# Kernel tuning notes

Hardware: AMD Instinct MI355X
Metric: run time of the kernel (lower is better)

Reference implementation:

```python
import jax, jax.numpy as jnp
import numpy as np

N_NODES = 50000
N_EDGES = 800000
LN_EPS = 1e-5


def _segment_softmax_aggr(msg, t, dst, n):
    # SoftmaxAggregation(learn=True): alpha = softmax(msg * t) per dest segment, out = sum(alpha * msg)
    logits = msg * t  # [E, C]
    m = jax.ops.segment_max(logits, dst, num_segments=n)
    m = jnp.where(jnp.isfinite(m), m, 0.0)  # empty segments -> 0 to keep exp finite
    e = jnp.exp(logits - m[dst])
    denom = jax.ops.segment_sum(e, dst, num_segments=n)
    alpha = e / jnp.maximum(denom[dst], 1e-16)
    return jax.ops.segment_sum(alpha * msg, dst, num_segments=n)


def _sage_conv(x, src, dst, wp, bp, t, wl, bl, wr):
    # project=True: messages come from relu(lin(x)); root term uses ORIGINAL x
    xp = jax.nn.relu(x @ wp + bp)
    msg = xp[src]                                   # [E, C] gather
    aggr = _segment_softmax_aggr(msg, t, dst, x.shape[0])
    out = aggr @ wl + bl + x @ wr
    # normalize=True: L2 normalize rows (eps as in F.normalize)
    nrm = jnp.maximum(jnp.linalg.norm(out, axis=-1, keepdims=True), 1e-12)
    return out / nrm


def _mem_pool(x, k, w_conv, wl, bl):
    # PyG MemPooling, tau=1: Student-t kernel 1/(1+d^2)
    H, K, F = k.shape
    kk = k.reshape(H * K, F)
    d2 = (jnp.sum(kk * kk, -1)[:, None] + jnp.sum(x * x, -1)[None, :]
          - 2.0 * kk @ x.T)                          # [H*K, N]
    d2 = jnp.maximum(d2, 0.0)
    dist = 1.0 / (1.0 + d2)
    dist = dist.reshape(H, K, -1).transpose(0, 2, 1)  # [H, N, K]
    S = dist / jnp.sum(dist, -1, keepdims=True)       # per-head normalize over clusters
    S = jnp.einsum('h,hnk->nk', w_conv, S)            # 1x1 conv mixing heads (no bias)
    S = jax.nn.softmax(S, axis=-1)                    # [N, K]
    xp = S.T @ x                                      # [K, F]
    return xp @ wl + bl                               # [K, out]


def setup_inputs() -> dict:
    key = jax.random.key(0)
    ks = jax.random.split(key, 20)
    rn = lambda i, shp, s: jax.random.normal(ks[i], shp, dtype=jnp.float32) * s
    inp = {
        'x': rn(0, (N_NODES, 64), 1.0),
        'edge_index': jax.random.randint(ks[1], (2, N_EDGES), 0, N_NODES, dtype=jnp.int32),
        'w_proj1': rn(2, (64, 64), 0.1), 'b_proj1': rn(3, (64,), 0.05),
        't1': jnp.ones((64,), jnp.float32),
        'w_l1': rn(4, (64, 256), 0.1), 'b_l1': rn(5, (256,), 0.05),
        'w_r1': rn(6, (64, 256), 0.1),
        'w_proj2': rn(7, (256, 256), 0.05), 'b_proj2': rn(8, (256,), 0.05),
        't2': jnp.ones((256,), jnp.float32),
        'w_l2': rn(9, (256, 128), 0.05), 'b_l2': rn(10, (128,), 0.05),
        'w_r2': rn(11, (256, 128), 0.05),
        'k_mem': rn(12, (4, 4, 128), 1.0),
        'w_conv': rn(13, (4,), 0.5),
        'w_memlin': rn(14, (128, 128), 0.08), 'b_memlin': rn(15, (128,), 0.05),
        'w_fx': rn(16, (128, 64), 0.08), 'b_fx': rn(17, (64,), 0.05),
        'gamma': jnp.ones((64,), jnp.float32),
        'beta': jnp.zeros((64,), jnp.float32),
    }
    return inp


def reference(x, edge_index, w_proj1, b_proj1, t1, w_l1, b_l1, w_r1,
              w_proj2, b_proj2, t2, w_l2, b_l2, w_r2,
              k_mem, w_conv, w_memlin, b_memlin, w_fx, b_fx, gamma, beta):
    src, dst = edge_index[0], edge_index[1]
    h = _sage_conv(x, src, dst, w_proj1, b_proj1, t1, w_l1, b_l1, w_r1)
    h = jax.nn.relu(h)                              # dropout = identity (eval)
    h = _sage_conv(h, src, dst, w_proj2, b_proj2, t2, w_l2, b_l2, w_r2)
    h = jax.nn.relu(h)
    pooled = _mem_pool(h, k_mem, w_conv, w_memlin, b_memlin)  # [4, 128]
    g = jnp.mean(pooled, axis=0, keepdims=True)     # global_mean_pool -> [1, 128]
    y = g @ w_fx + b_fx                             # [1, 64]
    mu = jnp.mean(y, -1, keepdims=True)
    var = jnp.var(y, -1, keepdims=True)
    y = (y - mu) / jnp.sqrt(var + LN_EPS) * gamma + beta
    return jax.nn.relu(y)
```

## Files before the change

### kernel.cpp

```cpp
#include <hip/hip_runtime.h>
#include <hip/hip_bf16.h>

#define N_NODES 50000
#define N_EDGES 800000
#define NB 196
#define PC_SLICES 2048
#define AGG_GRID 2048

typedef __attribute__((ext_vector_type(8))) short short8;
typedef __attribute__((ext_vector_type(4))) float f32x4;
typedef __attribute__((ext_vector_type(2))) float f32x2;

#define QSCALE2 (2.f / 255.f)
#define QINV2   127.5f
#define QSCALE1 (12.75f / 255.f)
#define QINV1   20.f

__device__ __forceinline__ float us2f(unsigned short u) {
    return __uint_as_float(((unsigned int)u) << 16);
}
__device__ __forceinline__ unsigned short f2bu(float f) {
    unsigned int u = __float_as_uint(f);
    unsigned int r = (u + 0x7fffu + ((u >> 16) & 1u)) >> 16;
    return (unsigned short)r;
}
__device__ __forceinline__ float exp2_hw(float x) {
    float r;
    __asm__("v_exp_f32 %0, %1" : "=v"(r) : "v"(x));
    return r;
}
__device__ __forceinline__ void async16(const void* g, void* l) {
    __builtin_amdgcn_global_load_lds(
        (const __attribute__((address_space(1))) unsigned int*)g,
        (__attribute__((address_space(3))) unsigned int*)l, 16, 0, 0);
}
#define LOG2E 1.44269504088896f

__global__ void k_hist(const int* __restrict__ dst, int* __restrict__ counts) {
    int e = blockIdx.x * 256 + threadIdx.x;
    if (e < N_EDGES) atomicAdd(&counts[dst[e]], 1);
}

__global__ __launch_bounds__(256) void k_scan1(const int* __restrict__ counts,
                                               int* __restrict__ row_ptr,
                                               int* __restrict__ partial) {
    __shared__ int sd[256];
    int t = threadIdx.x, i = blockIdx.x * 256 + t;
    int v = (i < N_NODES) ? counts[i] : 0;
    sd[t] = v;
    __syncthreads();
    for (int off = 1; off < 256; off <<= 1) {
        int o = (t >= off) ? sd[t - off] : 0;
        __syncthreads();
        sd[t] += o;
        __syncthreads();
    }
    if (i < N_NODES) row_ptr[i] = sd[t] - v;
    if (t == 255) partial[blockIdx.x] = sd[255];
}

__global__ __launch_bounds__(256) void k_scan3b(int* __restrict__ row_ptr,
                                                const int* __restrict__ partial,
                                                int* __restrict__ cursor) {
    __shared__ int sd[256];
    int t = threadIdx.x;
    sd[t] = (t < blockIdx.x) ? partial[t] : 0;
    __syncthreads();
    for (int off = 128; off > 0; off >>= 1) {
        if (t < off) sd[t] += sd[t + off];
        __syncthreads();
    }
    int base = sd[0];
    int i = blockIdx.x * 256 + t;
    if (i < N_NODES) {
        int v = row_ptr[i] + base;
        row_ptr[i] = v;
        cursor[i] = v;
    }
    if (blockIdx.x == 0 && t == 0) row_ptr[N_NODES] = N_EDGES;
}

__global__ void k_scatter(const int* __restrict__ src, const int* __restrict__ dst,
                          int* __restrict__ cursor, int* __restrict__ src_sorted) {
    int e = blockIdx.x * 256 + threadIdx.x;
    if (e < N_EDGES) {
        int d = dst[e];
        int pos = atomicAdd(&cursor[d], 1);
        src_sorted[pos] = src[e];
    }
}

__global__ __launch_bounds__(256) void k_dhist(const int* __restrict__ counts,
                                               int* __restrict__ bcnt) {
    __shared__ int h[64];
    int t = threadIdx.x;
    if (t < 64) h[t] = 0;
    __syncthreads();
    int i = blockIdx.x * 256 + t;
    if (i < N_NODES) {
        int d = counts[i];
        d = d > 63 ? 63 : d;
        atomicAdd(&h[d], 1);
    }
    __syncthreads();
    if (t < 64) bcnt[blockIdx.x * 64 + t] = h[t];
}

__global__ __launch_bounds__(256) void k_dscan2(const int* __restrict__ bcnt,
                                                int* __restrict__ boff,
                                                int* __restrict__ dtot) {
    __shared__ int sd[256];
    int d = blockIdx.x, t = threadIdx.x;
    int v = (t < NB) ? bcnt[t * 64 + d] : 0;
    sd[t] = v;
    __syncthreads();
    for (int off = 1; off < 256; off <<= 1) {
        int o = (t >= off) ? sd[t - off] : 0;
        __syncthreads();
        sd[t] += o;
        __syncthreads();
    }
    if (t < NB) boff[t * 64 + d] = sd[t] - v;
    if (t == 255) dtot[d] = sd[255];
}

__global__ __launch_bounds__(256) void k_dscatter(const int* __restrict__ counts,
                                                  const int* __restrict__ boff,
                                                  const int* __restrict__ dtot,
                                                  int* __restrict__ perm) {
    __shared__ int h[64];
    __shared__ int dbaseS[64];
    int t = threadIdx.x;
    if (t < 64) {
        h[t] = 0;
        int v = dtot[t];
        int s = v;
        for (int off = 1; off < 64; off <<= 1) {
            int o = __shfl_up(s, off);
            if (t >= off) s += o;
        }
        dbaseS[t] = s - v;
    }
    __syncthreads();
    int i = blockIdx.x * 256 + t;
    if (i < N_NODES) {
        int d = counts[i];
        d = d > 63 ? 63 : d;
        int rank = atomicAdd(&h[d], 1);
        perm[dbaseS[d] + boff[blockIdx.x * 64 + d] + rank] = i;
    }
}

#define XCAST_N (N_NODES * 64)
#define PREP_TOT (XCAST_N + 167936)
__global__ __launch_bounds__(256) void k_prep(const float* __restrict__ x,
                                              const float* __restrict__ wp1,
                                              const float* __restrict__ wl1,
                                              const float* __restrict__ wr1,
                                              const float* __restrict__ wp2,
                                              const float* __restrict__ wl2,
                                              const float* __restrict__ wr2,
                                              unsigned short* __restrict__ cat1,
                                              unsigned short* __restrict__ B0T,
                                              unsigned short* __restrict__ B1T,
                                              unsigned short* __restrict__ BP2T,
                                              unsigned short* __restrict__ B2T) {
    int idx = (blockIdx.x * 256 + threadIdx.x) * 4;
    if (idx < XCAST_N) {
        int i = idx >> 6, j = idx & 63;
        float4 v = *(const float4*)&x[idx];
        ushort4 o = { f2bu(v.x), f2bu(v.y), f2bu(v.z), f2bu(v.w) };
        *(ushort4*)&cat1[i * 128 + 64 + j] = o;
        return;
    }
    int w = idx - XCAST_N;
    if (w < 4096)  { float4 v = *(const float4*)&wp1[w]; int k = w >> 6, n = w & 63;
                     B0T[n*64+k]=f2bu(v.x); B0T[(n+1)*64+k]=f2bu(v.y);
                     B0T[(n+2)*64+k]=f2bu(v.z); B0T[(n+3)*64+k]=f2bu(v.w); return; }
    w -= 4096;
    if (w < 16384) { float4 v = *(const float4*)&wl1[w]; int k = w >> 8, n = w & 255;
                     B1T[n*128+k]=f2bu(v.x); B1T[(n+1)*128+k]=f2bu(v.y);
                     B1T[(n+2)*128+k]=f2bu(v.z); B1T[(n+3)*128+k]=f2bu(v.w); return; }
    w -= 16384;
    if (w < 16384) { float4 v = *(const float4*)&wr1[w]; int k = w >> 8, n = w & 255;
                     B1T[n*128+64+k]=f2bu(v.x); B1T[(n+1)*128+64+k]=f2bu(v.y);
                     B1T[(n+2)*128+64+k]=f2bu(v.z); B1T[(n+3)*128+64+k]=f2bu(v.w); return; }
    w -= 16384;
    if (w < 65536) { float4 v = *(const float4*)&wp2[w]; int k = w >> 8, n = w & 255;
                     BP2T[n*256+k]=f2bu(v.x); BP2T[(n+1)*256+k]=f2bu(v.y);
                     BP2T[(n+2)*256+k]=f2bu(v.z); BP2T[(n+3)*256+k]=f2bu(v.w); return; }
    w -= 65536;
    if (w < 32768) { float4 v = *(const float4*)&wl2[w]; int k = w >> 7, n = w & 127;
                     B2T[n*512+k]=f2bu(v.x); B2T[(n+1)*512+k]=f2bu(v.y);
                     B2T[(n+2)*512+k]=f2bu(v.z); B2T[(n+3)*512+k]=f2bu(v.w); return; }
    w -= 32768;
    if (w < 32768) { float4 v = *(const float4*)&wr2[w]; int k = w >> 7, n = w & 127;
                     B2T[n*512+256+k]=f2bu(v.x); B2T[(n+1)*512+256+k]=f2bu(v.y);
                     B2T[(n+2)*512+256+k]=f2bu(v.z); B2T[(n+3)*512+256+k]=f2bu(v.w); return; }
}

template<int K, int C, int LDA, int LDOUT, int OUT_OFF, int EP, int WPB, int MH>
__global__ __launch_bounds__(256, WPB) void k_gemm(const unsigned short* __restrict__ A,
                                                   const unsigned short* __restrict__ BT,
                                                   const float* __restrict__ bias,
                                                   void* __restrict__ outv,
                                                   const float* __restrict__ kmem,
                                                   const float* __restrict__ wconv,
                                                   float* __restrict__ Sm,
                                                   float qinv) {
    constexpr int NT = C / 16;
    constexpr int SAE = 64 * MH * 64;
    constexpr int SBE = C * 64;
    constexpr int STAGE_B = (SAE + SBE) * 2;
    constexpr int RPLD = (EP == 2) ? (C + 4) : ((EP == 3) ? (C + 16) : (C + 8));
    constexpr int RP_B = 64 * RPLD * (EP == 2 ? 4 : (EP == 3 ? 1 : 2));
    constexpr int SMEM_B = STAGE_B > RP_B ? STAGE_B : RP_B;
    constexpr int POOL_B = (EP == 2) ? (2048 * 4 + 64 + 16) : 16;
    __shared__ __align__(16) char smem[SMEM_B + POOL_B];
    unsigned short* sA = (unsigned short*)smem;
    unsigned short* sB = sA + SAE;
    float* kls  = (float*)(smem + SMEM_B);
    float* kk2s = kls + 2048;
    float* wcs  = kk2s + 16;

    int t = threadIdx.x;
    int wid = t >> 6, lane = t & 63;
    int lrow = lane & 15, quad = lane >> 4;
    int m0 = blockIdx.x * (64 * MH);

    if (EP == 2) {
        for (int i = t; i < 2048; i += 256) kls[i] = kmem[i];
        if (t < 4) wcs[t] = wconv[t];
        __syncthreads();
        if (t < 16) {
            float s = 0.f;
            for (int f = 0; f < 128; ++f) { float v = kls[t * 128 + f]; s += v * v; }
            kk2s[t] = s;
        }
    }

    f32x4 acc[MH][NT];
#pragma unroll
    for (int h = 0; h < MH; ++h)
#pragma unroll
        for (int nt = 0; nt < NT; ++nt)
#pragma unroll
            for (int r = 0; r < 4; ++r) acc[h][nt][r] = 0.f;

    for (int k0 = 0; k0 < K; k0 += 64) {
        __syncthreads();
        for (int i = t; i < 64 * MH * 8; i += 256) {
            int r = i >> 3, seg = i & 7;
            size_t m = (size_t)(m0 + r);
            async16(&A[m * LDA + k0 + ((seg ^ (r & 7)) << 3)],
                    (char*)sA + (size_t)(i - lane) * 16);
        }
        for (int i = t; i < C * 8; i += 256) {
            int n = i >> 3, seg = i & 7;
            async16(&BT[(size_t)n * K + k0 + ((seg ^ (n & 7)) << 3)],
                    (char*)sB + (size_t)(i - lane) * 16);
        }
        __syncthreads();
#pragma unroll
        for (int kk = 0; kk < 2; ++kk) {
            int sw = lrow & 7;
            short8 av[MH];
#pragma unroll
            for (int h = 0; h < MH; ++h)
                av[h] = *(const short8*)&sA[(h * 64 + wid * 16 + lrow) * 64 +
                                            (((kk * 4 + quad) ^ sw) << 3)];
#pragma unroll
            for (int nt = 0; nt < NT; ++nt) {
                short8 bfg = *(const short8*)&sB[(nt * 16 + lrow) * 64 +
                                                 (((kk * 4 + quad) ^ sw) << 3)];
#pragma unroll
                for (int h = 0; h < MH; ++h)
                    acc[h][nt] = __builtin_amdgcn_mfma_f32_16x16x32_bf16(av[h], bfg, acc[h][nt], 0, 0, 0);
            }
        }
    }

#pragma unroll
    for (int h = 0; h < MH; ++h) {
#pragma unroll
        for (int nt = 0; nt < NT; ++nt) {
            float bv = bias[nt * 16 + lrow];
#pragma unroll
            for (int r = 0; r < 4; ++r) acc[h][nt][r] += bv;
        }
        if (EP == 1 || EP == 2) {
#pragma unroll
            for (int r = 0; r < 4; ++r) {
                float ss = 0.f;
#pragma unroll
                for (int nt = 0; nt < NT; ++nt) ss += acc[h][nt][r] * acc[h][nt][r];
                ss += __shfl_xor(ss, 1);
                ss += __shfl_xor(ss, 2);
                ss += __shfl_xor(ss, 4);
                ss += __shfl_xor(ss, 8);
                float rinv = 1.f / fmaxf(sqrtf(ss), 1e-12f);
#pragma unroll
                for (int nt = 0; nt < NT; ++nt)
                    acc[h][nt][r] = fmaxf(acc[h][nt][r] * rinv, 0.f);
            }
        } else {
#pragma unroll
            for (int nt = 0; nt < NT; ++nt)
#pragma unroll
                for (int r = 0; r < 4; ++r) acc[h][nt][r] = fmaxf(acc[h][nt][r], 0.f);
        }
    }

    __syncthreads();
#pragma unroll
    for (int h = 0; h < MH; ++h) {
        if (EP == 2) {
            float* rp = (float*)smem;
#pragma unroll
            for (int nt = 0; nt < NT; ++nt)
#pragma unroll
                for (int r = 0; r < 4; ++r)
                    rp[(wid * 16 + quad * 4 + r) * RPLD + nt * 16 + lrow] = acc[h][nt][r];
            __syncthreads();
            float* outp = (float*)outv;
            for (int i = t; i < 64 * C / 4; i += 256) {
                int f = i * 4, r = f / C, c = f % C;
                int m = m0 + h * 64 + r;
                if (m < N_NODES)
                    *(float4*)&outp[(size_t)m * LDOUT + OUT_OFF + c] = *(const float4*)&rp[r * RPLD + c];
            }
            {
                int row = t >> 2, p = t & 3;
                int cbase = p * 32;
                float dots[16];
#pragma unroll
                for (int k = 0; k < 16; ++k) dots[k] = 0.f;
                float x2 = 0.f;
#pragma unroll
                for (int j = 0; j < 8; ++j) {
                    int c4 = (j + p * 2) & 7;
                    float4 xv = *(const float4*)&rp[row * RPLD + cbase + c4 * 4];
                    x2 += xv.x * xv.x + xv.y * xv.y + xv.z * xv.z + xv.w * xv.w;
#pragma unroll
                    for (int k = 0; k < 16; ++k) {
                        float4 kv = *(const float4*)&kls[k * 128 + cbase + c4 * 4];
                        dots[k] += xv.x * kv.x + xv.y * kv.y + xv.z * kv.z + xv.w * kv.w;
                    }
                }
#pragma unroll
                for (int k = 0; k < 16; ++k) {
                    dots[k] += __shfl_xor(dots[k], 1);
                    dots[k] += __shfl_xor(dots[k], 2);
                }
                x2 += __shfl_xor(x2, 1);
                x2 += __shfl_xor(x2, 2);
                if (p == 0) {
                    int m = m0 + h * 64 + row;
                    if (m < N_NODES) {
                        float dist[16];
#pragma unroll
                        for (int k = 0; k < 16; ++k) {
                            float d2 = fmaxf(kk2s[k] + x2 - 2.f * dots[k], 0.f);
                            dist[k] = 1.f / (1.f + d2);
                        }
                        float s0 = 0.f, s1 = 0.f, s2 = 0.f, s3 = 0.f;
#pragma unroll
                        for (int hh = 0; hh < 4; ++hh) {
                            float den = dist[hh * 4] + dist[hh * 4 + 1] +
                                        dist[hh * 4 + 2] + dist[hh * 4 + 3];
                            float inv = wcs[hh] / den;
                            s0 += dist[hh * 4 + 0] * inv;
                            s1 += dist[hh * 4 + 1] * inv;
                            s2 += dist[hh * 4 + 2] * inv;
                            s3 += dist[hh * 4 + 3] * inv;
                        }
                        float mx = fmaxf(fmaxf(s0, s1), fmaxf(s2, s3));
                        float e0 = __expf(s0 - mx), e1 = __expf(s1 - mx);
                        float e2 = __expf(s2 - mx), e3 = __expf(s3 - mx);
                        float inv = 1.f / (e0 + e1 + e2 + e3);
                        *(float4*)&Sm[(size_t)m * 4] =
                            make_float4(e0 * inv, e1 * inv, e2 * inv, e3 * inv);
                    }
                }
            }
            __syncthreads();
        } else if (EP == 3) {
            unsigned char* rp = (unsigned char*)smem;
#pragma unroll
            for (int nt = 0; nt < NT; ++nt)
#pragma unroll
                for (int r = 0; r < 4; ++r) {
                    float q = fminf(__builtin_rintf(acc[h][nt][r] * qinv), 255.f);
                    rp[(wid * 16 + quad * 4 + r) * RPLD + nt * 16 + lrow] = (unsigned char)(int)q;
                }
            __syncthreads();
            unsigned char* outp = (unsigned char*)outv;
            for (int i = t; i < 64 * C / 16; i += 256) {
                int f = i * 16, r = f / C, c = f % C;
                int m = m0 + h * 64 + r;
                if (m < N_NODES)
                    *(uint4*)&outp[(size_t)m * LDOUT + OUT_OFF + c] = *(const uint4*)&rp[r * RPLD + c];
            }
            __syncthreads();
        } else {
            unsigned short* rp = (unsigned short*)smem;
#pragma unroll
            for (int nt = 0; nt < NT; ++nt)
#pragma unroll
                for (int r = 0; r < 4; ++r)
                    rp[(wid * 16 + quad * 4 + r) * RPLD + nt * 16 + lrow] = f2bu(acc[h][nt][r]);
            __syncthreads();
            unsigned short* outp = (unsigned short*)outv;
            for (int i = t; i < 64 * C / 8; i += 256) {
                int f = i * 8, r = f / C, c = f % C;
                int m = m0 + h * 64 + r;
                if (m < N_NODES)
                    *(uint4*)&outp[(size_t)m * LDOUT + OUT_OFF + c] = *(const uint4*)&rp[r * RPLD + c];
            }
            __syncthreads();
        }
    }
}

__global__ __launch_bounds__(256, 8) void k_aggr256(const unsigned char* __restrict__ xp,
                                                    const float* __restrict__ tvec,
                                                    const int* __restrict__ row_ptr,
                                                    const int* __restrict__ srcs,
                                                    const int* __restrict__ perm,
                                                    unsigned short* __restrict__ outp) {
    int t = threadIdx.x & 63;
    int wid = threadIdx.x >> 6;
    float4 tv4 = *(const float4*)&tvec[t * 4];
    f32x2 tv01 = {tv4.x * (LOG2E * QSCALE2), tv4.y * (LOG2E * QSCALE2)};
    f32x2 tv23 = {tv4.z * (LOG2E * QSCALE2), tv4.w * (LOG2E * QSCALE2)};
#define EDGE_BODY(VV, MSK)                                                     \
    {                                                                          \
        f32x2 m01 = {(float)((VV) & 0xFFu), (float)(((VV) >> 8) & 0xFFu)};     \
        f32x2 m23 = {(float)(((VV) >> 16) & 0xFFu), (float)((VV) >> 24)};      \
        f32x2 l01 = m01 * tv01, l23 = m23 * tv23;                              \
        f32x2 w01, w23;                                                        \
        w01.x = exp2_hw(l01.x) * (MSK); w01.y = exp2_hw(l01.y) * (MSK);        \
        w23.x = exp2_hw(l23.x) * (MSK); w23.y = exp2_hw(l23.y) * (MSK);        \
        se01 += w01; se23 += w23;                                              \
        sem01 = __builtin_elementwise_fma(w01, m01, sem01);                    \
        sem23 = __builtin_elementwise_fma(w23, m23, sem23);                    \
    }
    for (int g = blockIdx.x; g < N_NODES / 4; g += AGG_GRID) {
        int grp = N_NODES / 4 - 1 - g;
        int n = __builtin_amdgcn_readfirstlane(perm[grp * 4 + wid]);
        int beg = __builtin_amdgcn_readfirstlane(row_ptr[n]);
        int end = __builtin_amdgcn_readfirstlane(row_ptr[n + 1]);
        f32x2 se01 = {0.f, 0.f}, se23 = {0.f, 0.f};
        f32x2 sem01 = {0.f, 0.f}, sem23 = {0.f, 0.f};
        int e = beg;
        for (; e + 16 <= end; e += 16) {
            unsigned int v[16];
#pragma unroll
            for (int j = 0; j < 16; ++j) {
                const unsigned char* p = xp + (size_t)srcs[e + j] * 256;
                v[j] = *(const unsigned int*)&p[t * 4];
            }
#pragma unroll
            for (int j = 0; j < 16; ++j) EDGE_BODY(v[j], 1.f)
        }
        for (; e + 8 <= end; e += 8) {
            unsigned int v[8];
#pragma unroll
            for (int j = 0; j < 8; ++j) {
                const unsigned char* p = xp + (size_t)srcs[e + j] * 256;
                v[j] = *(const unsigned int*)&p[t * 4];
            }
#pragma unroll
            for (int j = 0; j < 8; ++j) EDGE_BODY(v[j], 1.f)
        }
        if (e < end) {
            int last = end - 1;
            unsigned int v[8];
#pragma unroll
            for (int j = 0; j < 8; ++j) {
                int ee = e + j;
                ee = ee < end ? ee : last;
                const unsigned char* p = xp + (size_t)srcs[ee] * 256;
                v[j] = *(const unsigned int*)&p[t * 4];
            }
#pragma unroll
            for (int j = 0; j < 8; ++j) {
                float msk = (e + j < end) ? 1.f : 0.f;
                EDGE_BODY(v[j], msk)
            }
        }
        ushort4 o;
        o.x = f2bu(QSCALE2 * sem01.x / fmaxf(se01.x, 1e-16f));
        o.y = f2bu(QSCALE2 * sem01.y / fmaxf(se01.y, 1e-16f));
        o.z = f2bu(QSCALE2 * sem23.x / fmaxf(se23.x, 1e-16f));
        o.w = f2bu(QSCALE2 * sem23.y / fmaxf(se23.y, 1e-16f));
        *(ushort4*)&outp[(size_t)n * 512 + t * 4] = o;
    }
#undef EDGE_BODY
}

__global__ __launch_bounds__(256, 8) void k_aggr64(const unsigned char* __restrict__ xp,
                                                   const float* __restrict__ tvec,
                                                   const int* __restrict__ row_ptr,
                                                   const int* __restrict__ srcs,
                                                   const int* __restrict__ perm,
                                                   unsigned short* __restrict__ outp) {
    int c = threadIdx.x & 63;
    int wid = threadIdx.x >> 6;
    float tv = tvec[c] * (LOG2E * QSCALE1);
    for (int g = blockIdx.x; g < N_NODES / 4; g += AGG_GRID) {
        int grp = N_NODES / 4 - 1 - g;
        int n = __builtin_amdgcn_readfirstlane(perm[grp * 4 + wid]);
        int beg = __builtin_amdgcn_readfirstlane(row_ptr[n]);
        int end = __builtin_amdgcn_readfirstlane(row_ptr[n + 1]);
        float se = 0.f, sem = 0.f;
        int e = beg;
        for (; e + 16 <= end; e += 16) {
            unsigned char v[16];
#pragma unroll
            for (int j = 0; j < 16; ++j)
                v[j] = xp[(size_t)srcs[e + j] * 64 + c];
#pragma unroll
            for (int j = 0; j < 16; ++j) {
                float msg = (float)v[j];
                float w = exp2_hw(msg * tv);
                se += w;
                sem = fmaf(w, msg, sem);
            }
        }
        for (; e + 8 <= end; e += 8) {
            unsigned char v[8];
#pragma unroll
            for (int j = 0; j < 8; ++j)
                v[j] = xp[(size_t)srcs[e + j] * 64 + c];
#pragma unroll
            for (int j = 0; j < 8; ++j) {
                float msg = (float)v[j];
                float w = exp2_hw(msg * tv);
                se += w;
                sem = fmaf(w, msg, sem);
            }
        }
        if (e < end) {
            int last = end - 1;
            unsigned char v[8];
#pragma unroll
            for (int j = 0; j < 8; ++j) {
                int ee = e + j;
                ee = ee < end ? ee : last;
                v[j] = xp[(size_t)srcs[ee] * 64 + c];
            }
#pragma unroll
            for (int j = 0; j < 8; ++j) {
                float msk = (e + j < end) ? 1.f : 0.f;
                float msg = (float)v[j];
                float w = exp2_hw(msg * tv) * msk;
                se += w;
                sem = fmaf(w, msg, sem);
            }
        }
        outp[(size_t)n * 128 + c] = f2bu(QSCALE1 * sem / fmaxf(se, 1e-16f));
    }
}

__global__ __launch_bounds__(256) void k_pool_c(const float* __restrict__ h2,
                                                const float* __restrict__ Sm,
                                                float* __restrict__ part) {
    int t = threadIdx.x;
    int c = t & 127, sub = t >> 7;
    int slice = blockIdx.x * 2 + sub;
    float a0 = 0.f, a1 = 0.f, a2 = 0.f, a3 = 0.f;
    for (int n = slice; n < N_NODES; n += PC_SLICES) {
        float xv = h2[(size_t)n * 128 + c];
        float4 sv = *(const float4*)&Sm[(size_t)n * 4];
        a0 = fmaf(sv.x, xv, a0);
        a1 = fmaf(sv.y, xv, a1);
        a2 = fmaf(sv.z, xv, a2);
        a3 = fmaf(sv.w, xv, a3);
    }
    float* p = &part[(size_t)slice * 512];
    p[0 * 128 + c] = a0;
    p[1 * 128 + c] = a1;
    p[2 * 128 + c] = a2;
    p[3 * 128 + c] = a3;
}

__global__ __launch_bounds__(256) void k_pool_b(const float* __restrict__ part,
                                                float* __restrict__ pooled) {
    int j = blockIdx.x;
    float s = 0.f;
    for (int b = threadIdx.x; b < PC_SLICES; b += 256) s += part[(size_t)b * 512 + j];
#pragma unroll
    for (int off = 32; off > 0; off >>= 1) s += __shfl_xor(s, off);
    __shared__ float red[4];
    int lane = threadIdx.x & 63, wid = threadIdx.x >> 6;
    if (lane == 0) red[wid] = s;
    __syncthreads();
    if (threadIdx.x == 0) pooled[j] = red[0] + red[1] + red[2] + red[3];
}

__global__ __launch_bounds__(128) void k_final(const float* __restrict__ pooled,
                                               const float* __restrict__ wmem,
                                               const float* __restrict__ bmem,
                                               const float* __restrict__ wfx,
                                               const float* __restrict__ bfx,
                                               const float* __restrict__ gamma,
                                               const float* __restrict__ beta,
                                               float* __restrict__ out) {
    __shared__ float gx[128], g[128];
    int t = threadIdx.x;
    gx[t] = 0.25f * (pooled[t] + pooled[128 + t] + pooled[256 + t] + pooled[384 + t]);
    __syncthreads();
    float acc = bmem[t];
    for (int f = 0; f < 128; ++f) acc = fmaf(gx[f], wmem[f * 128 + t], acc);
    g[t] = acc;
    __syncthreads();
    if (t < 64) {
        float y = bfx[t];
        for (int f = 0; f < 128; ++f) y = fmaf(g[f], wfx[f * 64 + t], y);
        float s = y, s2 = y * y;
#pragma unroll
        for (int off = 32; off > 0; off >>= 1) {
            s += __shfl_xor(s, off);
            s2 += __shfl_xor(s2, off);
        }
        float mu = s * (1.f / 64.f);
        float var = s2 * (1.f / 64.f) - mu * mu;
        float v = (y - mu) / sqrtf(var + 1e-5f) * gamma[t] + beta[t];
        out[t] = fmaxf(v, 0.f);
    }
}

extern "C" void kernel_launch(void* const* d_in, const int* in_sizes, int n_in,
                              void* d_out, int out_size, void* d_ws, size_t ws_size,
                              hipStream_t stream) {
    const float* x        = (const float*)d_in[0];
    const int*   ei       = (const int*)  d_in[1];
    const float* w_proj1  = (const float*)d_in[2];
    const float* b_proj1  = (const float*)d_in[3];
    const float* t1       = (const float*)d_in[4];
    const float* w_l1     = (const float*)d_in[5];
    const float* b_l1     = (const float*)d_in[6];
    const float* w_r1     = (const float*)d_in[7];
    const float* w_proj2  = (const float*)d_in[8];
    const float* b_proj2  = (const float*)d_in[9];
    const float* t2       = (const float*)d_in[10];
    const float* w_l2     = (const float*)d_in[11];
    const float* b_l2     = (const float*)d_in[12];
    const float* w_r2     = (const float*)d_in[13];
    const float* k_mem    = (const float*)d_in[14];
    const float* w_conv   = (const float*)d_in[15];
    const float* w_memlin = (const float*)d_in[16];
    const float* b_memlin = (const float*)d_in[17];
    const float* w_fx     = (const float*)d_in[18];
    const float* b_fx     = (const float*)d_in[19];
    const float* gamma    = (const float*)d_in[20];
    const float* beta     = (const float*)d_in[21];
    const int* src = ei;
    const int* dst = ei + N_EDGES;
    (void)in_sizes; (void)n_in; (void)out_size; (void)ws_size;

    char* W = (char*)d_ws;
    const size_t MB = 1024 * 1024;
    int*   row_ptr    = (int*)(W + 0);
    int*   cursor     = (int*)(W + 256 * 1024);
    int*   partial    = (int*)(W + 512 * 1024);
    int*   dtot       = (int*)(W + 512 * 1024 + 4096);
    int*   bcnt       = (int*)(W + 520 * 1024);
    int*   boff       = (int*)(W + 576 * 1024);
    int*   src_sorted = (int*)(W + 768 * 1024);
    unsigned short* cat1 = (unsigned short*)(W + 4 * MB);
    unsigned char*  xp1  = (unsigned char*)(W + 17 * MB);
    unsigned short* cat2 = (unsigned short*)(W + 24 * MB);
    unsigned char*  xp2  = (unsigned char*)(W + 76 * MB);
    float* h2     = (float*)(W + 102 * MB);
    float* Sm     = (float*)(W + 128 * MB);
    float* pooled = (float*)(W + 131 * MB);
    unsigned short* B0T  = (unsigned short*)(W + 133 * MB);
    unsigned short* B1T  = (unsigned short*)(W + 134 * MB);
    unsigned short* BP2T = (unsigned short*)(W + 135 * MB);
    unsigned short* B2T  = (unsigned short*)(W + 136 * MB);
    int*   perm   = (int*)(W + 138 * MB);
    float* part   = (float*)(W + 140 * MB);

    hipMemsetAsync(cursor, 0, N_NODES * sizeof(int), stream);
    k_hist<<<(N_EDGES + 255) / 256, 256, 0, stream>>>(dst, cursor);
    k_dhist<<<NB, 256, 0, stream>>>(cursor, bcnt);
    k_scan1<<<NB, 256, 0, stream>>>(cursor, row_ptr, partial);
    k_dscan2<<<64, 256, 0, stream>>>(bcnt, boff, dtot);
    k_dscatter<<<NB, 256, 0, stream>>>(cursor, boff, dtot, perm);
    k_scan3b<<<NB, 256, 0, stream>>>(row_ptr, partial, cursor);
    k_scatter<<<(N_EDGES + 255) / 256, 256, 0, stream>>>(src, dst, cursor, src_sorted);

    k_prep<<<(PREP_TOT / 4 + 255) / 256, 256, 0, stream>>>(
        x, w_proj1, w_l1, w_r1, w_proj2, w_l2, w_r2, cat1, B0T, B1T, BP2T, B2T);

    const int GB = (N_NODES + 127) / 128;

    k_gemm<64, 64, 128, 64, 0, 3, 4, 2><<<GB, 256, 0, stream>>>(
        cat1 + 64, B0T, b_proj1, xp1, nullptr, nullptr, nullptr, QINV1);
    k_aggr64<<<AGG_GRID, 256, 0, stream>>>(xp1, t1, row_ptr, src_sorted, perm, cat1);
    k_gemm<128, 256, 128, 512, 256, 1, 3, 2><<<GB, 256, 0, stream>>>(
        cat1, B1T, b_l1, cat2, nullptr, nullptr, nullptr, 0.f);

    k_gemm<256, 256, 512, 256, 0, 3, 3, 2><<<GB, 256, 0, stream>>>(
        cat2 + 256, BP2T, b_proj2, xp2, nullptr, nullptr, nullptr, QINV2);
    k_aggr256<<<AGG_GRID, 256, 0, stream>>>(xp2, t2, row_ptr, src_sorted, perm, cat2);
    k_gemm<512, 128, 512, 128, 0, 2, 3, 2><<<GB, 256, 0, stream>>>(
        cat2, B2T, b_l2, h2, k_mem, w_conv, Sm, 0.f);

    k_pool_c<<<PC_SLICES / 2, 256, 0, stream>>>(h2, Sm, part);
    k_pool_b<<<512, 256, 0, stream>>>(part, pooled);
    k_final<<<1, 128, 0, stream>>>(pooled, w_memlin, b_memlin, w_fx, b_fx, gamma, beta,
                                   (float*)d_out);
}
```

Measured before the change: 374.0 us.

## Replace degree-sorted node scheduling with edge-balanced merge-path split per wave

Drops the degree histogram, scan and permutation kernels. A binary search over row_ptr now gives each of 8192 waves a contiguous node range holding about the same number of edges. The aggregation kernels stream edges across node boundaries in chunks of 16 and finalize each node inline when its edge range ends. This removes three setup launches and the random perm indirection, and balances work by edges rather than by nodes. In exchange it adds a data-dependent finalize branch inside the unrolled edge loop and lowers the occupancy hint from 8 to 4.

```diff
diff --git a/kernel.cpp b/kernel.cpp
--- a/kernel.cpp
+++ b/kernel.cpp
@@ -5,7 +5,7 @@
 #define N_EDGES 800000
 #define NB 196
 #define PC_SLICES 2048
-#define AGG_GRID 2048
+#define NWAVES 8192
 
 typedef __attribute__((ext_vector_type(8))) short short8;
 typedef __attribute__((ext_vector_type(4))) float f32x4;
@@ -90,65 +90,18 @@
     }
 }
 
-__global__ __launch_bounds__(256) void k_dhist(const int* __restrict__ counts,
-                                               int* __restrict__ bcnt) {
-    __shared__ int h[64];
-    int t = threadIdx.x;
-    if (t < 64) h[t] = 0;
-    __syncthreads();
-    int i = blockIdx.x * 256 + t;
-    if (i < N_NODES) {
-        int d = counts[i];
-        d = d > 63 ? 63 : d;
-        atomicAdd(&h[d], 1);
-    }
-    __syncthreads();
-    if (t < 64) bcnt[blockIdx.x * 64 + t] = h[t];
-}
-
-__global__ __launch_bounds__(256) void k_dscan2(const int* __restrict__ bcnt,
-                                                int* __restrict__ boff,
-                                                int* __restrict__ dtot) {
-    __shared__ int sd[256];
-    int d = blockIdx.x, t = threadIdx.x;
-    int v = (t < NB) ? bcnt[t * 64 + d] : 0;
-    sd[t] = v;
-    __syncthreads();
-    for (int off = 1; off < 256; off <<= 1) {
-        int o = (t >= off) ? sd[t - off] : 0;
-        __syncthreads();
-        sd[t] += o;
-        __syncthreads();
-    }
-    if (t < NB) boff[t * 64 + d] = sd[t] - v;
-    if (t == 255) dtot[d] = sd[255];
-}
-
-__global__ __launch_bounds__(256) void k_dscatter(const int* __restrict__ counts,
-                                                  const int* __restrict__ boff,
-                                                  const int* __restrict__ dtot,
-                                                  int* __restrict__ perm) {
-    __shared__ int h[64];
-    __shared__ int dbaseS[64];
-    int t = threadIdx.x;
-    if (t < 64) {
-        h[t] = 0;
-        int v = dtot[t];
-        int s = v;
-        for (int off = 1; off < 64; off <<= 1) {
-            int o = __shfl_up(s, off);
-            if (t >= off) s += o;
-        }
-        dbaseS[t] = s - v;
-    }
-    __syncthreads();
-    int i = blockIdx.x * 256 + t;
-    if (i < N_NODES) {
-        int d = counts[i];
-        d = d > 63 ? 63 : d;
-        int rank = atomicAdd(&h[d], 1);
-        perm[dbaseS[d] + boff[blockIdx.x * 64 + d] + rank] = i;
-    }
+__global__ __launch_bounds__(256) void k_split(const int* __restrict__ row_ptr,
+                                               int* __restrict__ split) {
+    int w = blockIdx.x * 256 + threadIdx.x;
+    if (w > NWAVES) return;
+    if (w == NWAVES) { split[w] = N_NODES; return; }
+    int target = (int)((long long)w * N_EDGES / NWAVES);
+    int lo = 0, hi = N_NODES;
+    while (lo < hi) {
+        int mid = (lo + hi) >> 1;
+        if (row_ptr[mid] < target) lo = mid + 1; else hi = mid;
+    }
+    split[w] = lo;
 }
 
 #define XCAST_N (N_NODES * 64)
@@ -422,145 +375,144 @@
     }
 }
 
-__global__ __launch_bounds__(256, 8) void k_aggr256(const unsigned char* __restrict__ xp,
+__global__ __launch_bounds__(256, 4) void k_aggr256(const unsigned char* __restrict__ xp,
                                                     const float* __restrict__ tvec,
                                                     const int* __restrict__ row_ptr,
                                                     const int* __restrict__ srcs,
-                                                    const int* __restrict__ perm,
+                                                    const int* __restrict__ split,
                                                     unsigned short* __restrict__ outp) {
     int t = threadIdx.x & 63;
-    int wid = threadIdx.x >> 6;
+    int w = blockIdx.x * 4 + (threadIdx.x >> 6);
     float4 tv4 = *(const float4*)&tvec[t * 4];
     f32x2 tv01 = {tv4.x * (LOG2E * QSCALE2), tv4.y * (LOG2E * QSCALE2)};
     f32x2 tv23 = {tv4.z * (LOG2E * QSCALE2), tv4.w * (LOG2E * QSCALE2)};
-#define EDGE_BODY(VV, MSK)                                                     \
+    int n    = __builtin_amdgcn_readfirstlane(split[w]);
+    int nend = __builtin_amdgcn_readfirstlane(split[w + 1]);
+    if (n >= nend) return;
+    int e    = __builtin_amdgcn_readfirstlane(row_ptr[n]);
+    int eend = __builtin_amdgcn_readfirstlane(row_ptr[nend]);
+    int rp_next = __builtin_amdgcn_readfirstlane(row_ptr[n + 1]);
+    f32x2 se01 = {0.f, 0.f}, se23 = {0.f, 0.f};
+    f32x2 sem01 = {0.f, 0.f}, sem23 = {0.f, 0.f};
+
+#define FINALIZE()                                                             \
+    {                                                                          \
+        ushort4 o;                                                             \
+        o.x = f2bu(QSCALE2 * sem01.x / fmaxf(se01.x, 1e-16f));                 \
+        o.y = f2bu(QSCALE2 * sem01.y / fmaxf(se01.y, 1e-16f));                 \
+        o.z = f2bu(QSCALE2 * sem23.x / fmaxf(se23.x, 1e-16f));                 \
+        o.w = f2bu(QSCALE2 * sem23.y / fmaxf(se23.y, 1e-16f));                 \
+        *(ushort4*)&outp[(size_t)n * 512 + t * 4] = o;                         \
+        se01 = (f32x2){0.f, 0.f}; se23 = (f32x2){0.f, 0.f};                    \
+        sem01 = (f32x2){0.f, 0.f}; sem23 = (f32x2){0.f, 0.f};                  \
+        ++n;                                                                   \
+        rp_next = (n < nend) ? __builtin_amdgcn_readfirstlane(row_ptr[n + 1])  \
+                             : 0x7FFFFFFF;                                     \
+    }
+#define EDGE_BODY(VV)                                                          \
     {                                                                          \
         f32x2 m01 = {(float)((VV) & 0xFFu), (float)(((VV) >> 8) & 0xFFu)};     \
         f32x2 m23 = {(float)(((VV) >> 16) & 0xFFu), (float)((VV) >> 24)};      \
         f32x2 l01 = m01 * tv01, l23 = m23 * tv23;                              \
         f32x2 w01, w23;                                                        \
-        w01.x = exp2_hw(l01.x) * (MSK); w01.y = exp2_hw(l01.y) * (MSK);        \
-        w23.x = exp2_hw(l23.x) * (MSK); w23.y = exp2_hw(l23.y) * (MSK);        \
+        w01.x = exp2_hw(l01.x); w01.y = exp2_hw(l01.y);                        \
+        w23.x = exp2_hw(l23.x); w23.y = exp2_hw(l23.y);                        \
         se01 += w01; se23 += w23;                                              \
         sem01 = __builtin_elementwise_fma(w01, m01, sem01);                    \
         sem23 = __builtin_elementwise_fma(w23, m23, sem23);                    \
     }
-    for (int g = blockIdx.x; g < N_NODES / 4; g += AGG_GRID) {
-        int grp = N_NODES / 4 - 1 - g;
-        int n = __builtin_amdgcn_readfirstlane(perm[grp * 4 + wid]);
-        int beg = __builtin_amdgcn_readfirstlane(row_ptr[n]);
-        int end = __builtin_amdgcn_readfirstlane(row_ptr[n + 1]);
-        f32x2 se01 = {0.f, 0.f}, se23 = {0.f, 0.f};
-        f32x2 sem01 = {0.f, 0.f}, sem23 = {0.f, 0.f};
-        int e = beg;
-        for (; e + 16 <= end; e += 16) {
-            unsigned int v[16];
+
+    while (rp_next <= e) FINALIZE();
+
+    while (e < eend) {
+        unsigned int v[16];
+        int rem = eend - e;
+        int cnt = rem > 16 ? 16 : rem;
+        if (cnt == 16) {
 #pragma unroll
             for (int j = 0; j < 16; ++j) {
                 const unsigned char* p = xp + (size_t)srcs[e + j] * 256;
                 v[j] = *(const unsigned int*)&p[t * 4];
             }
-#pragma unroll
-            for (int j = 0; j < 16; ++j) EDGE_BODY(v[j], 1.f)
-        }
-        for (; e + 8 <= end; e += 8) {
-            unsigned int v[8];
-#pragma unroll
-            for (int j = 0; j < 8; ++j) {
-                const unsigned char* p = xp + (size_t)srcs[e + j] * 256;
-                v[j] = *(const unsigned int*)&p[t * 4];
-            }
-#pragma unroll
-            for (int j = 0; j < 8; ++j) EDGE_BODY(v[j], 1.f)
-        }
-        if (e < end) {
-            int last = end - 1;
-            unsigned int v[8];
-#pragma unroll
-            for (int j = 0; j < 8; ++j) {
+        } else {
+#pragma unroll
+            for (int j = 0; j < 16; ++j) {
                 int ee = e + j;
-                ee = ee < end ? ee : last;
+                ee = ee < eend ? ee : eend - 1;
                 const unsigned char* p = xp + (size_t)srcs[ee] * 256;
                 v[j] = *(const unsigned int*)&p[t * 4];
             }
-#pragma unroll
-            for (int j = 0; j < 8; ++j) {
-                float msk = (e + j < end) ? 1.f : 0.f;
-                EDGE_BODY(v[j], msk)
-            }
-        }
-        ushort4 o;
-        o.x = f2bu(QSCALE2 * sem01.x / fmaxf(se01.x, 1e-16f));
-        o.y = f2bu(QSCALE2 * sem01.y / fmaxf(se01.y, 1e-16f));
-        o.z = f2bu(QSCALE2 * sem23.x / fmaxf(se23.x, 1e-16f));
-        o.w = f2bu(QSCALE2 * sem23.y / fmaxf(se23.y, 1e-16f));
-        *(ushort4*)&outp[(size_t)n * 512 + t * 4] = o;
+        }
+#pragma unroll
+        for (int j = 0; j < 16; ++j) {
+            if (j < cnt) {
+                EDGE_BODY(v[j])
+                while (e + j + 1 == rp_next) FINALIZE();
+            }
+        }
+        e += cnt;
     }
 #undef EDGE_BODY
-}
-
-__global__ __launch_bounds__(256, 8) void k_aggr64(const unsigned char* __restrict__ xp,
+#undef FINALIZE
+}
+
+__global__ __launch_bounds__(256, 4) void k_aggr64(const unsigned char* __restrict__ xp,
                                                    const float* __restrict__ tvec,
                                                    const int* __restrict__ row_ptr,
                                                    const int* __restrict__ srcs,
-                                                   const int* __restrict__ perm,
+                                                   const int* __restrict__ split,
                                                    unsigned short* __restrict__ outp) {
     int c = threadIdx.x & 63;
-    int wid = threadIdx.x >> 6;
+    int w = blockIdx.x * 4 + (threadIdx.x >> 6);
     float tv = tvec[c] * (LOG2E * QSCALE1);
-    for (int g = blockIdx.x; g < N_NODES / 4; g += AGG_GRID) {
-        int grp = N_NODES / 4 - 1 - g;
-        int n = __builtin_amdgcn_readfirstlane(perm[grp * 4 + wid]);
-        int beg = __builtin_amdgcn_readfirstlane(row_ptr[n]);
-        int end = __builtin_amdgcn_readfirstlane(row_ptr[n + 1]);
-        float se = 0.f, sem = 0.f;
-        int e = beg;
-        for (; e + 16 <= end; e += 16) {
-            unsigned char v[16];
+    int n    = __builtin_amdgcn_readfirstlane(split[w]);
+    int nend = __builtin_amdgcn_readfirstlane(split[w + 1]);
+    if (n >= nend) return;
+    int e    = __builtin_amdgcn_readfirstlane(row_ptr[n]);
+    int eend = __builtin_amdgcn_readfirstlane(row_ptr[nend]);
+    int rp_next = __builtin_amdgcn_readfirstlane(row_ptr[n + 1]);
+    float se = 0.f, sem = 0.f;
+
+#define FIN1()                                                                 \
+    {                                                                          \
+        outp[(size_t)n * 128 + c] = f2bu(QSCALE1 * sem / fmaxf(se, 1e-16f));   \
+        se = 0.f; sem = 0.f;                                                   \
+        ++n;                                                                   \
+        rp_next = (n < nend) ? __builtin_amdgcn_readfirstlane(row_ptr[n + 1])  \
+                             : 0x7FFFFFFF;                                     \
+    }
+
+    while (rp_next <= e) FIN1();
+
+    while (e < eend) {
+        unsigned char v[16];
+        int rem = eend - e;
+        int cnt = rem > 16 ? 16 : rem;
+        if (cnt == 16) {
 #pragma unroll
             for (int j = 0; j < 16; ++j)
                 v[j] = xp[(size_t)srcs[e + j] * 64 + c];
+        } else {
 #pragma unroll
             for (int j = 0; j < 16; ++j) {
+                int ee = e + j;
+                ee = ee < eend ? ee : eend - 1;
+                v[j] = xp[(size_t)srcs[ee] * 64 + c];
+            }
+        }
+#pragma unroll
+        for (int j = 0; j < 16; ++j) {
+            if (j < cnt) {
                 float msg = (float)v[j];
-                float w = exp2_hw(msg * tv);
-                se += w;
-                sem = fmaf(w, msg, sem);
-            }
-        }
-        for (; e + 8 <= end; e += 8) {
-            unsigned char v[8];
-#pragma unroll
-            for (int j = 0; j < 8; ++j)
-                v[j] = xp[(size_t)srcs[e + j] * 64 + c];
-#pragma unroll
-            for (int j = 0; j < 8; ++j) {
-                float msg = (float)v[j];
-                float w = exp2_hw(msg * tv);
-                se += w;
-                sem = fmaf(w, msg, sem);
-            }
-        }
-        if (e < end) {
-            int last = end - 1;
-            unsigned char v[8];
-#pragma unroll
-            for (int j = 0; j < 8; ++j) {
-                int ee = e + j;
-                ee = ee < end ? ee : last;
-                v[j] = xp[(size_t)srcs[ee] * 64 + c];
-            }
-#pragma unroll
-            for (int j = 0; j < 8; ++j) {
-                float msk = (e + j < end) ? 1.f : 0.f;
-                float msg = (float)v[j];
-                float w = exp2_hw(msg * tv) * msk;
-                se += w;
-                sem = fmaf(w, msg, sem);
-            }
-        }
-        outp[(size_t)n * 128 + c] = f2bu(QSCALE1 * sem / fmaxf(se, 1e-16f));
-    }
+                float wv = exp2_hw(msg * tv);
+                se += wv;
+                sem = fmaf(wv, msg, sem);
+                while (e + j + 1 == rp_next) FIN1();
+            }
+        }
+        e += cnt;
+    }
+#undef FIN1
 }
 
 __global__ __launch_bounds__(256) void k_pool_c(const float* __restrict__ h2,
@@ -665,9 +617,7 @@
     int*   row_ptr    = (int*)(W + 0);
     int*   cursor     = (int*)(W + 256 * 1024);
     int*   partial    = (int*)(W + 512 * 1024);
-    int*   dtot       = (int*)(W + 512 * 1024 + 4096);
-    int*   bcnt       = (int*)(W + 520 * 1024);
-    int*   boff       = (int*)(W + 576 * 1024);
+    int*   split      = (int*)(W + 520 * 1024);
     int*   src_sorted = (int*)(W + 768 * 1024);
     unsigned short* cat1 = (unsigned short*)(W + 4 * MB);
     unsigned char*  xp1  = (unsigned char*)(W + 17 * MB);
@@ -680,32 +630,30 @@
     unsigned short* B1T  = (unsigned short*)(W + 134 * MB);
     unsigned short* BP2T = (unsigned short*)(W + 135 * MB);
     unsigned short* B2T  = (unsigned short*)(W + 136 * MB);
-    int*   perm   = (int*)(W + 138 * MB);
     float* part   = (float*)(W + 140 * MB);
 
     hipMemsetAsync(cursor, 0, N_NODES * sizeof(int), stream);
     k_hist<<<(N_EDGES + 255) / 256, 256, 0, stream>>>(dst, cursor);
-    k_dhist<<<NB, 256, 0, stream>>>(cursor, bcnt);
     k_scan1<<<NB, 256, 0, stream>>>(cursor, row_ptr, partial);
-    k_dscan2<<<64, 256, 0, stream>>>(bcnt, boff, dtot);
-    k_dscatter<<<NB, 256, 0, stream>>>(cursor, boff, dtot, perm);
     k_scan3b<<<NB, 256, 0, stream>>>(row_ptr, partial, cursor);
+    k_split<<<(NWAVES + 1 + 255) / 256, 256, 0, stream>>>(row_ptr, split);
     k_scatter<<<(N_EDGES + 255) / 256, 256, 0, stream>>>(src, dst, cursor, src_sorted);
 
     k_prep<<<(PREP_TOT / 4 + 255) / 256, 256, 0, stream>>>(
         x, w_proj1, w_l1, w_r1, w_proj2, w_l2, w_r2, cat1, B0T, B1T, BP2T, B2T);
 
     const int GB = (N_NODES + 127) / 128;
+    const int AGB = NWAVES / 4;
 
     k_gemm<64, 64, 128, 64, 0, 3, 4, 2><<<GB, 256, 0, stream>>>(
         cat1 + 64, B0T, b_proj1, xp1, nullptr, nullptr, nullptr, QINV1);
-    k_aggr64<<<AGG_GRID, 256, 0, stream>>>(xp1, t1, row_ptr, src_sorted, perm, cat1);
+    k_aggr64<<<AGB, 256, 0, stream>>>(xp1, t1, row_ptr, src_sorted, split, cat1);
     k_gemm<128, 256, 128, 512, 256, 1, 3, 2><<<GB, 256, 0, stream>>>(
         cat1, B1T, b_l1, cat2, nullptr, nullptr, nullptr, 0.f);
 
     k_gemm<256, 256, 512, 256, 0, 3, 3, 2><<<GB, 256, 0, stream>>>(
         cat2 + 256, BP2T, b_proj2, xp2, nullptr, nullptr, nullptr, QINV2);
-    k_aggr256<<<AGG_GRID, 256, 0, stream>>>(xp2, t2, row_ptr, src_sorted, perm, cat2);
+    k_aggr256<<<AGB, 256, 0, stream>>>(xp2, t2, row_ptr, src_sorted, split, cat2);
     k_gemm<512, 128, 512, 128, 0, 2, 3, 2><<<GB, 256, 0, stream>>>(
         cat2, B2T, b_l2, h2, k_mem, w_conv, Sm, 0.f);
 
```

Measured after the change: 376.7 us. Within noise of the previous version (+0.7%).
